# Optimization experiments

Measured on AMD Instinct MI355X. Metric: run time of the kernel, lower is better.

Reference implementation:

```python
import jax, jax.numpy as jnp
import numpy as np

N_HEADS = 32
N_KV_HEADS = 8
HEAD_DIM = 128
HIDDEN = 4096
ROPE_BASE = 10000.0


def _rope_tables(seq_len, head_dim, base):
    inv_freq = 1.0 / (base ** (jnp.arange(0, head_dim, 2, dtype=jnp.float32) / head_dim))
    t = jnp.arange(seq_len, dtype=jnp.float32)
    freqs = jnp.outer(t, inv_freq)                    # (S, D/2)
    emb = jnp.concatenate([freqs, freqs], axis=-1)    # (S, D)
    return jnp.cos(emb), jnp.sin(emb)


def _rotate_half(x):
    half = x.shape[-1] // 2
    return jnp.concatenate([-x[..., half:], x[..., :half]], axis=-1)


def _apply_rope(x, cos, sin):
    # x: (B, H, S, D); cos/sin: (S, D)
    return x * cos[None, None] + _rotate_half(x) * sin[None, None]


def setup_inputs() -> dict:
    key = jax.random.key(0)
    k1, k2, k3 = jax.random.split(key, 3)
    bsz, q_len = 2, 2048
    total_heads = N_HEADS + 2 * N_KV_HEADS
    hidden_states = jax.random.normal(k1, (bsz, q_len, HIDDEN), dtype=jnp.float32)
    w_qkv = jax.random.normal(k2, (total_heads * HEAD_DIM, HIDDEN), dtype=jnp.float32) * 0.02
    w_o = jax.random.normal(k3, (HIDDEN, N_HEADS * HEAD_DIM), dtype=jnp.float32) * 0.02
    return {"hidden_states": hidden_states, "w_qkv": w_qkv, "w_o": w_o}


def reference(hidden_states, w_qkv, w_o):
    bsz, q_len, _ = hidden_states.shape
    n_rep = N_HEADS // N_KV_HEADS

    qkv = jnp.einsum('bsh,oh->bso', hidden_states, w_qkv)  # (B, S, total_heads*D)
    q_sz = N_HEADS * HEAD_DIM
    kv_sz = N_KV_HEADS * HEAD_DIM
    q = qkv[..., :q_sz].reshape(bsz, q_len, N_HEADS, HEAD_DIM).transpose(0, 2, 1, 3)
    k = qkv[..., q_sz:q_sz + kv_sz].reshape(bsz, q_len, N_KV_HEADS, HEAD_DIM).transpose(0, 2, 1, 3)
    v = qkv[..., q_sz + kv_sz:].reshape(bsz, q_len, N_KV_HEADS, HEAD_DIM).transpose(0, 2, 1, 3)

    cos, sin = _rope_tables(q_len, HEAD_DIM, ROPE_BASE)
    q = _apply_rope(q, cos, sin)
    k = _apply_rope(k, cos, sin)

    # repeat KV heads for GQA
    k = jnp.repeat(k, n_rep, axis=1)  # (B, H, S, D)
    v = jnp.repeat(v, n_rep, axis=1)

    scale = HEAD_DIM ** -0.5
    scores = jnp.einsum('bhqd,bhkd->bhqk', q, k) * scale
    causal = jnp.tril(jnp.ones((q_len, q_len), dtype=bool))
    scores = jnp.where(causal[None, None], scores, jnp.finfo(scores.dtype).min)
    attn = jax.nn.softmax(scores, axis=-1)
    out = jnp.einsum('bhqk,bhkd->bhqd', attn, v)  # (B, H, S, D)
    out = out.transpose(0, 2, 1, 3).reshape(bsz, q_len, N_HEADS * HEAD_DIM)
    return jnp.einsum('bso,ho->bsh', out, w_o)
```

## Files before the change

kernel.cpp:

```cpp
#include <hip/hip_runtime.h>
#include <stdint.h>

#define N_HEADS   32
#define N_KV      8
#define HEAD_DIM  128
#define HIDDEN_DIM 4096
#define BSZ       2
#define SEQ       2048
#define TOT_HEADS 48
#define QKV_DIM   6144
#define ROWS      4096
#define ROPE_HEADS 40

typedef __attribute__((ext_vector_type(4)))  float f32x4;
typedef __attribute__((ext_vector_type(16))) float f32x16;
typedef __attribute__((ext_vector_type(8)))  short bf16x8;
typedef unsigned short u16;
typedef unsigned int   u32;

#define AS1 __attribute__((address_space(1)))
#define AS3 __attribute__((address_space(3)))

static __device__ __forceinline__ float bf16f(u16 u) { return __uint_as_float(((u32)u) << 16); }
static __device__ __forceinline__ u16 f2bf(float f) {
  u32 x = __float_as_uint(f);
  x += 0x7fffu + ((x >> 16) & 1u);
  return (u16)(x >> 16);
}
static __device__ __forceinline__ u32 cvt_pk_bf16(float lo, float hi) {
  u32 r;
  asm("v_cvt_pk_bf16_f32 %0, %1, %2" : "=v"(r) : "v"(lo), "v"(hi));
  return r;
}
static __device__ __forceinline__ bf16x8 mk8(u32 a, u32 b, u32 c, u32 d) {
  union { u32 u[4]; bf16x8 v; } x;
  x.u[0] = a; x.u[1] = b; x.u[2] = c; x.u[3] = d;
  return x.v;
}

#define SBAR()  do { __builtin_amdgcn_sched_barrier(0); __builtin_amdgcn_s_barrier(); \
                     __builtin_amdgcn_sched_barrier(0); } while (0)
#define LGKM0() do { asm volatile("s_waitcnt lgkmcnt(0)" ::: "memory"); \
                     __builtin_amdgcn_sched_barrier(0); } while (0)

__global__ void cast3_k(const float4* __restrict__ a, const float4* __restrict__ b,
                        const float4* __restrict__ c,
                        ushort4* __restrict__ oa, ushort4* __restrict__ ob,
                        ushort4* __restrict__ oc, int na, int nb, int nc) {
  int i = blockIdx.x * blockDim.x + threadIdx.x;
  const int stride = gridDim.x * blockDim.x;
  const int tot = na + nb + nc;
  for (; i < tot; i += stride) {
    const float4* s; ushort4* d; int j = i;
    if (j < na)           { s = a; d = oa; }
    else if (j < na + nb) { s = b; d = ob; j -= na; }
    else                  { s = c; d = oc; j -= na + nb; }
    const float4 v = s[j];
    ushort4 o;
    o.x = f2bf(v.x); o.y = f2bf(v.y); o.z = f2bf(v.z); o.w = f2bf(v.w);
    d[j] = o;
  }
}

__global__ void rope_tables_k(float* __restrict__ ctab, float* __restrict__ stab) {
  int t = blockIdx.x * blockDim.x + threadIdx.x;
  if (t >= SEQ * 64) return;
  int s = t >> 6, i = t & 63;
  float inv = powf(10000.0f, -(float)i / 64.0f);
  float ang = (float)s * inv;
  float sv, cv;
  sincosf(ang, &sv, &cv);
  ctab[t] = cv; stab[t] = sv;
}

template<int F32OUT>
__global__ __launch_bounds__(512, 2)
void gemm256_k(const u16* __restrict__ A, const u16* __restrict__ Bw,
               void* __restrict__ C, int M, int N, int K)
{
  extern __shared__ uint4 lds[];
  uint4* LA = lds;
  uint4* LB = lds + 4096;
  const int NT = K >> 6;
  const int tid  = threadIdx.x;
  const int lane = tid & 63;
  const int wave = tid >> 6;
  const int nbx = N >> 8;
  const int cpx = gridDim.x >> 3;
  const int wg  = (blockIdx.x & 7) * cpx + (blockIdx.x >> 3);
  const int bm = (wg / nbx) << 8;
  const int bn = (wg % nbx) << 8;

  const int wm = (wave >> 2) << 7;
  const int wn = (wave & 3) << 6;
  const int fr = lane & 15;
  const int fq = lane >> 4;
  const int s7 = fr & 7;

  const int rA  = (wave << 3) + (lane >> 3);
  const int c8e = (((lane & 7) ^ (lane >> 3)) << 3);

  auto SA = [&](int t, int h, int buf) {
    uint4* d = LA + (buf << 11) + (h << 10) + (wave << 6);
    const u16* s = A + (size_t)(bm + (h << 7) + rA) * K + (t << 6) + c8e;
    __builtin_amdgcn_global_load_lds((const AS1 u32*)s, (AS3 u32*)d, 16, 0, 0);
    __builtin_amdgcn_global_load_lds((const AS1 u32*)(s + (size_t)64 * K), (AS3 u32*)(d + 512), 16, 0, 0);
  };
  auto SB = [&](int t, int h, int buf) {
    uint4* d = LB + (buf << 11) + (h << 10) + (wave << 6);
    const u16* s = Bw + (size_t)(bn + (h << 7) + rA) * K + (t << 6) + c8e;
    __builtin_amdgcn_global_load_lds((const AS1 u32*)s, (AS3 u32*)d, 16, 0, 0);
    __builtin_amdgcn_global_load_lds((const AS1 u32*)(s + (size_t)64 * K), (AS3 u32*)(d + 512), 16, 0, 0);
  };

  f32x4 acc[8][4];
#pragma unroll
  for (int m = 0; m < 8; ++m)
#pragma unroll
    for (int n = 0; n < 4; ++n)
      acc[m][n] = {0.f, 0.f, 0.f, 0.f};

  SB(0, 0, 0); SB(0, 1, 0); SA(0, 0, 0); SA(0, 1, 0);
  SB(1, 0, 1); SB(1, 1, 1); SA(1, 0, 1);
  asm volatile("s_waitcnt vmcnt(6)" ::: "memory");
  SBAR();

  bf16x8 Af[4][2], B0[2][2], B1[2][2];

#pragma unroll 1
  for (int t = 0; t < NT; ++t) {
    const int buf  = t & 1;
    const int base = buf << 11;
    const int abase = base + ((wm + fr) << 3);
    const int bbase = base + ((wn + fr) << 3);

#pragma unroll
    for (int m = 0; m < 4; ++m)
#pragma unroll
      for (int kk = 0; kk < 2; ++kk)
        Af[m][kk] = *reinterpret_cast<const bf16x8*>(&LA[abase + m * 128 + (((kk << 2) + fq) ^ s7)]);
#pragma unroll
    for (int n = 0; n < 2; ++n)
#pragma unroll
      for (int kk = 0; kk < 2; ++kk)
        B0[n][kk] = *reinterpret_cast<const bf16x8*>(&LB[bbase + n * 128 + (((kk << 2) + fq) ^ s7)]);
    if (t + 1 < NT) SA(t + 1, 1, buf ^ 1);
    SBAR();
    LGKM0();
    __builtin_amdgcn_s_setprio(1);
#pragma unroll
    for (int m = 0; m < 4; ++m)
#pragma unroll
      for (int n = 0; n < 2; ++n)
#pragma unroll
        for (int kk = 0; kk < 2; ++kk)
          acc[m][n] = __builtin_amdgcn_mfma_f32_16x16x32_bf16(Af[m][kk], B0[n][kk], acc[m][n], 0, 0, 0);
    __builtin_amdgcn_s_setprio(0);
    SBAR();

#pragma unroll
    for (int n = 0; n < 2; ++n)
#pragma unroll
      for (int kk = 0; kk < 2; ++kk)
        B1[n][kk] = *reinterpret_cast<const bf16x8*>(&LB[bbase + (2 + n) * 128 + (((kk << 2) + fq) ^ s7)]);
    SBAR();
    LGKM0();
    __builtin_amdgcn_s_setprio(1);
#pragma unroll
    for (int m = 0; m < 4; ++m)
#pragma unroll
      for (int n = 0; n < 2; ++n)
#pragma unroll
        for (int kk = 0; kk < 2; ++kk)
          acc[m][2 + n] = __builtin_amdgcn_mfma_f32_16x16x32_bf16(Af[m][kk], B1[n][kk], acc[m][2 + n], 0, 0, 0);
    __builtin_amdgcn_s_setprio(0);
    SBAR();

#pragma unroll
    for (int m = 0; m < 4; ++m)
#pragma unroll
      for (int kk = 0; kk < 2; ++kk)
        Af[m][kk] = *reinterpret_cast<const bf16x8*>(&LA[abase + 512 + m * 128 + (((kk << 2) + fq) ^ s7)]);
    if (t + 2 < NT) SB(t + 2, 0, buf);
    SBAR();
    LGKM0();
    __builtin_amdgcn_s_setprio(1);
#pragma unroll
    for (int m = 0; m < 4; ++m)
#pragma unroll
      for (int n = 0; n < 2; ++n)
#pragma unroll
        for (int kk = 0; kk < 2; ++kk)
          acc[4 + m][2 + n] = __builtin_amdgcn_mfma_f32_16x16x32_bf16(Af[m][kk], B1[n][kk], acc[4 + m][2 + n], 0, 0, 0);
    __builtin_amdgcn_s_setprio(0);
    SBAR();

    if (t + 2 < NT) { SB(t + 2, 1, buf); SA(t + 2, 0, buf); }
    __builtin_amdgcn_s_setprio(1);
#pragma unroll
    for (int m = 0; m < 4; ++m)
#pragma unroll
      for (int n = 0; n < 2; ++n)
#pragma unroll
        for (int kk = 0; kk < 2; ++kk)
          acc[4 + m][n] = __builtin_amdgcn_mfma_f32_16x16x32_bf16(Af[m][kk], B0[n][kk], acc[4 + m][n], 0, 0, 0);
    __builtin_amdgcn_s_setprio(0);
    if (t < NT - 2)       { asm volatile("s_waitcnt vmcnt(6)" ::: "memory"); }
    else if (t == NT - 2) { asm volatile("s_waitcnt vmcnt(0)" ::: "memory"); }
    SBAR();
  }

  const int col0 = bn + wn + fr;
#pragma unroll
  for (int m = 0; m < 8; ++m) {
#pragma unroll
    for (int i = 0; i < 4; ++i) {
      const int row = bm + wm + (m << 4) + (fq << 2) + i;
      if (F32OUT) {
        float* rp = reinterpret_cast<float*>(C) + (size_t)row * N + col0;
#pragma unroll
        for (int n = 0; n < 4; ++n) rp[n << 4] = acc[m][n][i];
      } else {
        u16* rp = reinterpret_cast<u16*>(C) + (size_t)row * N + col0;
#pragma unroll
        for (int n = 0; n < 4; ++n) rp[n << 4] = f2bf(acc[m][n][i]);
      }
    }
  }
}

__global__ void rope_scatter_k(const u16* __restrict__ QKV,
                               const float* __restrict__ ctab, const float* __restrict__ stab,
                               u16* __restrict__ Qo, u16* __restrict__ Ko)
{
  const int t = blockIdx.x * blockDim.x + threadIdx.x;
  const int d = t & 63;
  const int hh = (t >> 6) % ROPE_HEADS;
  const int row = t / (64 * ROPE_HEADS);
  const int b = row >> 11, sq = row & (SEQ - 1);
  const u16* src = QKV + (size_t)row * QKV_DIM + hh * HEAD_DIM;
  const float x1 = bf16f(src[d]);
  const float x2 = bf16f(src[d + 64]);
  const float c = ctab[(sq << 6) + d], sn = stab[(sq << 6) + d];
  float y1 = x1 * c - x2 * sn;
  float y2 = x2 * c + x1 * sn;
  u16* dst;
  if (hh < N_HEADS) {
    const float SC2 = 0.1275170747f;
    y1 *= SC2; y2 *= SC2;
    dst = Qo + ((size_t)(b * N_HEADS + hh) * SEQ + sq) * HEAD_DIM;
  } else {
    dst = Ko + ((size_t)(b * N_KV + (hh - N_HEADS)) * SEQ + sq) * HEAD_DIM;
  }
  dst[d] = f2bf(y1);
  dst[d + 64] = f2bf(y2);
}

__global__ __launch_bounds__(256)
void vtrans_k(const u16* __restrict__ QKV, u16* __restrict__ Vt)
{
  __shared__ u16 tile[64][72];
  const int idx = blockIdx.x;
  const int dt = idx & 1;
  const int st = (idx >> 1) & 31;
  const int kv = (idx >> 6) & 7;
  const int b  = idx >> 9;
  const int tid = threadIdx.x;
  const int s0 = st << 6, d0 = dt << 6;
  const int rl = tid >> 3, cc8 = (tid & 7) << 3;
#pragma unroll
  for (int p = 0; p < 2; ++p) {
    const int sl = rl + (p << 5);
    const u16* src = QKV + (size_t)(b * SEQ + s0 + sl) * QKV_DIM
                   + (N_HEADS + N_KV + kv) * HEAD_DIM + d0 + cc8;
    *reinterpret_cast<uint4*>(&tile[sl][cc8]) = *reinterpret_cast<const uint4*>(src);
  }
  __syncthreads();
#pragma unroll
  for (int p = 0; p < 2; ++p) {
    const int dl = rl + (p << 5);
    u16 tmp[8];
#pragma unroll
    for (int k2 = 0; k2 < 8; ++k2) tmp[k2] = tile[cc8 + k2][dl];
    u16* dst = Vt + ((size_t)(b * N_KV + kv) * HEAD_DIM + d0 + dl) * SEQ + s0 + cc8;
    *reinterpret_cast<uint4*>(dst) = *reinterpret_cast<const uint4*>(tmp);
  }
}

__global__ __launch_bounds__(512, 2)
void attn_mfma_k(const u16* __restrict__ Q, const u16* __restrict__ K,
                 const u16* __restrict__ Vt, u16* __restrict__ Out)
{
  __shared__ uint4 Ksm[2][512];
  __shared__ uint4 Vsm[2][512];
  const int tid  = threadIdx.x;
  const int lane = tid & 63;
  const int w    = tid >> 6;
  const int idx  = blockIdx.x;
  const int kvh  = idx & 7;
  const int b    = (idx >> 3) & 1;
  const int qi   = 31 - (idx >> 4);
  const int q0   = qi << 6;
  const int head = w & 3;
  const int qsub = w >> 2;
  const int h    = (kvh << 2) + head;
  const int diag = 2 * qi + qsub;
  const int nsub = 2 * qi + 2;

  const int ql = lane & 31;
  const int hh = lane >> 5;

  const u16* Qh = Q  + (size_t)(b * N_HEADS + h) * SEQ * HEAD_DIM;
  const u16* Kb = K  + (size_t)(b * N_KV + kvh) * SEQ * HEAD_DIM;
  const u16* Vb = Vt + (size_t)(b * N_KV + kvh) * HEAD_DIM * SEQ;

  int koff[8];
#pragma unroll
  for (int f = 0; f < 8; ++f) koff[f] = (ql << 4) + (((f << 1) + hh) ^ (ql & 15));
  int voff0[4], voff1[4];
#pragma unroll
  for (int dblk = 0; dblk < 4; ++dblk) {
    const int d = (dblk << 5) + ql;
    voff0[dblk] = (d << 2) + (hh ^ (d & 3));
    voff1[dblk] = (d << 2) + ((2 + hh) ^ (d & 3));
  }

  auto stage = [&](int buf, int ks) {
    const int sl = (w << 6) + lane;
    {
      const int row = sl >> 4, cs = sl & 15;
      const int g = cs ^ (row & 15);
      const u16* src = Kb + (size_t)(ks + row) * HEAD_DIM + (g << 3);
      __builtin_amdgcn_global_load_lds((const AS1 u32*)src, (AS3 u32*)&Ksm[buf][w << 6], 16, 0, 0);
    }
    {
      const int d = sl >> 2, cs = sl & 3;
      const int g = cs ^ (d & 3);
      const u16* src = Vb + (size_t)d * SEQ + ks + (g << 3);
      __builtin_amdgcn_global_load_lds((const AS1 u32*)src, (AS3 u32*)&Vsm[buf][w << 6], 16, 0, 0);
    }
  };

  bf16x8 qf[8];
#pragma unroll
  for (int f = 0; f < 8; ++f)
    qf[f] = *reinterpret_cast<const bf16x8*>(Qh + (size_t)(q0 + (qsub << 5) + ql) * HEAD_DIM
                                             + 16 * f + 8 * hh);

  f32x16 o[4];
#pragma unroll
  for (int dblk = 0; dblk < 4; ++dblk)
#pragma unroll
    for (int r = 0; r < 16; ++r) o[dblk][r] = 0.f;
  float m2 = -1e30f, lsum = 0.f;

  stage(0, 0);

#pragma unroll 1
  for (int s = 0; s < nsub; ++s) {
    const int cur = s & 1;
    __syncthreads();
    if (s + 1 < nsub) stage(cur ^ 1, (s + 1) << 5);

    if (s <= diag) {
      f32x16 T;
#pragma unroll
      for (int r = 0; r < 16; ++r) T[r] = 0.f;
      __builtin_amdgcn_s_setprio(1);
#pragma unroll
      for (int f = 0; f < 8; ++f) {
        const bf16x8 kf = *reinterpret_cast<const bf16x8*>(&Ksm[cur][koff[f]]);
        T = __builtin_amdgcn_mfma_f32_32x32x16_bf16(kf, qf[f], T, 0, 0, 0);
      }
      __builtin_amdgcn_s_setprio(0);

      if (s == diag) {
#pragma unroll
        for (int r = 0; r < 16; ++r) {
          const int kr = (r & 3) + ((r >> 2) << 3) + (hh << 2);
          if (kr > ql) T[r] = -1e30f;
        }
      }
      float mt = T[0];
#pragma unroll
      for (int r = 1; r < 16; ++r) mt = fmaxf(mt, T[r]);
      mt = fmaxf(mt, __shfl_xor(mt, 32));

      if (__any(mt > m2 + 8.f)) {
        const float mnew = fmaxf(m2, mt);
        const float resc = exp2f(m2 - mnew);
        lsum *= resc;
#pragma unroll
        for (int r = 0; r < 16; ++r) {
          const int qr = (r & 3) + ((r >> 2) << 3) + (hh << 2);
          const float rr = __shfl(resc, qr);
#pragma unroll
          for (int dblk = 0; dblk < 4; ++dblk) o[dblk][r] *= rr;
        }
        m2 = mnew;
      }

      float ps = 0.f;
#pragma unroll
      for (int r = 0; r < 16; ++r) { const float pv = exp2f(T[r] - m2); T[r] = pv; ps += pv; }
      ps += __shfl_xor(ps, 32);
      lsum += ps;

      u32 pk[8], sw[8];
#pragma unroll
      for (int i = 0; i < 8; ++i) {
        pk[i] = cvt_pk_bf16(T[2 * i], T[2 * i + 1]);
        sw[i] = (u32)__shfl_xor((int)pk[i], 32);
      }
      const bf16x8 a0 = hh ? mk8(sw[2], sw[3], pk[2], pk[3])
                           : mk8(pk[0], pk[1], sw[0], sw[1]);
      const bf16x8 a1 = hh ? mk8(sw[6], sw[7], pk[6], pk[7])
                           : mk8(pk[4], pk[5], sw[4], sw[5]);

      __builtin_amdgcn_s_setprio(1);
#pragma unroll
      for (int dblk = 0; dblk < 4; ++dblk) {
        const bf16x8 va = *reinterpret_cast<const bf16x8*>(&Vsm[cur][voff0[dblk]]);
        o[dblk] = __builtin_amdgcn_mfma_f32_32x32x16_bf16(a0, va, o[dblk], 0, 0, 0);
        const bf16x8 vb2 = *reinterpret_cast<const bf16x8*>(&Vsm[cur][voff1[dblk]]);
        o[dblk] = __builtin_amdgcn_mfma_f32_32x32x16_bf16(a1, vb2, o[dblk], 0, 0, 0);
      }
      __builtin_amdgcn_s_setprio(0);
    }
  }

  u16* Ob = Out + (size_t)(b * SEQ + q0 + (qsub << 5)) * HIDDEN_DIM + h * HEAD_DIM + ql;
#pragma unroll
  for (int r = 0; r < 16; ++r) {
    const int qr = (r & 3) + ((r >> 2) << 3) + (hh << 2);
    const float il = 1.0f / __shfl(lsum, qr);
    u16* rp = Ob + (size_t)qr * HIDDEN_DIM;
#pragma unroll
    for (int dblk = 0; dblk < 4; ++dblk)
      rp[dblk * 32] = f2bf(o[dblk][r] * il);
  }
}

extern "C" void kernel_launch(void* const* d_in, const int* in_sizes, int n_in,
                              void* d_out, int out_size, void* d_ws, size_t ws_size,
                              hipStream_t stream)
{
  const float* hs   = (const float*)d_in[0];
  const float* wqkv = (const float*)d_in[1];
  const float* wo   = (const float*)d_in[2];
  float* out = (float*)d_out;
  char* ws = (char*)d_ws;
  size_t off = 0;
  auto alloc = [&](size_t bytes) -> void* {
    void* p = ws + off;
    off += (bytes + 255) & ~(size_t)255;
    return p;
  };
  u16* Xbf    = (u16*)alloc((size_t)ROWS * HIDDEN_DIM * 2);
  u16* Wqkvbf = (u16*)alloc((size_t)QKV_DIM * HIDDEN_DIM * 2);
  u16* Wobf   = (u16*)alloc((size_t)HIDDEN_DIM * HIDDEN_DIM * 2);
  u16* QKVbf  = (u16*)alloc((size_t)ROWS * QKV_DIM * 2);
  u16* Qbf    = (u16*)alloc((size_t)BSZ * N_HEADS * SEQ * HEAD_DIM * 2);
  u16* Kbf    = (u16*)alloc((size_t)BSZ * N_KV * SEQ * HEAD_DIM * 2);
  u16* Vtbf   = (u16*)alloc((size_t)BSZ * N_KV * SEQ * HEAD_DIM * 2);
  float* ctab = (float*)alloc((size_t)SEQ * 64 * 4);
  float* stab = (float*)alloc((size_t)SEQ * 64 * 4);
  u16* AOut   = (u16*)alloc((size_t)ROWS * HIDDEN_DIM * 2);
  if (off > ws_size) return;

  (void)hipFuncSetAttribute(reinterpret_cast<const void*>(&gemm256_k<0>),
                            hipFuncAttributeMaxDynamicSharedMemorySize, 131072);
  (void)hipFuncSetAttribute(reinterpret_cast<const void*>(&gemm256_k<1>),
                            hipFuncAttributeMaxDynamicSharedMemorySize, 131072);

  cast3_k<<<4096, 256, 0, stream>>>((const float4*)hs, (const float4*)wqkv, (const float4*)wo,
                                    (ushort4*)Xbf, (ushort4*)Wqkvbf, (ushort4*)Wobf,
                                    ROWS * HIDDEN_DIM / 4, QKV_DIM * HIDDEN_DIM / 4,
                                    HIDDEN_DIM * HIDDEN_DIM / 4);
  rope_tables_k<<<(SEQ * 64) / 256, 256, 0, stream>>>(ctab, stab);

  gemm256_k<0><<<(ROWS / 256) * (QKV_DIM / 256), 512, 131072, stream>>>(Xbf, Wqkvbf, (void*)QKVbf,
                                                                        ROWS, QKV_DIM, HIDDEN_DIM);
  rope_scatter_k<<<ROWS * ROPE_HEADS * 64 / 256, 256, 0, stream>>>(QKVbf, ctab, stab, Qbf, Kbf);
  vtrans_k<<<BSZ * N_KV * (SEQ / 64) * (HEAD_DIM / 64), 256, 0, stream>>>(QKVbf, Vtbf);
  attn_mfma_k<<<BSZ * N_KV * (SEQ / 64), 512, 0, stream>>>(Qbf, Kbf, Vtbf, AOut);
  gemm256_k<1><<<(ROWS / 256) * (HIDDEN_DIM / 256), 512, 131072, stream>>>(AOut, Wobf, (void*)out,
                                                                           ROWS, HIDDEN_DIM, HIDDEN_DIM);
}
```

Baseline: 545.6 us.

## Use a 128x128-tile single-buffered GEMM kernel for the QKV projection

Adds a new bf16 MFMA GEMM with 128x128 tiles, 256 threads, static 32KB shared memory, XOR-swizzled LDS and direct global-to-LDS loads. The QKV projection now uses it in place of the 256x256-tile kernel. This yields more workgroups (1536 vs 384) for better CU occupancy on the 4096x6144 output. In exchange it loses the larger kernel's data reuse and any double-buffering, with a sync after each K step.

```diff
diff --git a/kernel.cpp b/kernel.cpp
--- a/kernel.cpp
+++ b/kernel.cpp
@@ -71,6 +71,89 @@
   float sv, cv;
   sincosf(ang, &sv, &cv);
   ctab[t] = cv; stab[t] = sv;
+}
+
+template<int F32OUT>
+__global__ __launch_bounds__(256, 2)
+void gemm_bt_k(const u16* __restrict__ A, const u16* __restrict__ Bw,
+               void* __restrict__ C, int M, int N, int K)
+{
+  __shared__ uint4 smA[1024];
+  __shared__ uint4 smB[1024];
+  const int tid = threadIdx.x;
+  const int nbx = N >> 7;
+  const int cpx = gridDim.x >> 3;
+  const int wg  = (blockIdx.x & 7) * cpx + (blockIdx.x >> 3);
+  const int bm = (wg / nbx) << 7;
+  const int bn = (wg % nbx) << 7;
+  const int lane = tid & 63;
+  const int wave = tid >> 6;
+  const int wm = (wave >> 1) << 6;
+  const int wn = (wave & 1) << 6;
+  const int fr = lane & 15;
+  const int fq = lane >> 4;
+
+  f32x4 acc[4][4];
+#pragma unroll
+  for (int i = 0; i < 4; ++i)
+#pragma unroll
+    for (int j = 0; j < 4; ++j)
+      acc[i][j] = {0.f, 0.f, 0.f, 0.f};
+
+  const int gl_r = lane >> 3;
+  const int gl_c = (lane & 7) ^ gl_r;
+
+  for (int k0 = 0; k0 < K; k0 += 64) {
+#pragma unroll
+    for (int i = 0; i < 4; ++i) {
+      const int rbase = (wave << 5) + (i << 3);
+      const int row = rbase + gl_r;
+      const u16* gA = A  + (size_t)(bm + row) * K + k0 + (gl_c << 3);
+      const u16* gB = Bw + (size_t)(bn + row) * K + k0 + (gl_c << 3);
+      __builtin_amdgcn_global_load_lds((const AS1 u32*)gA, (AS3 u32*)&smA[rbase << 3], 16, 0, 0);
+      __builtin_amdgcn_global_load_lds((const AS1 u32*)gB, (AS3 u32*)&smB[rbase << 3], 16, 0, 0);
+    }
+    __syncthreads();
+#pragma unroll
+    for (int kk = 0; kk < 2; ++kk) {
+      bf16x8 af[4], bfr[4];
+      const int cc = (kk << 2) + fq;
+#pragma unroll
+      for (int m = 0; m < 4; ++m) {
+        const int row = wm + (m << 4) + fr;
+        af[m] = *reinterpret_cast<const bf16x8*>(&smA[(row << 3) + (cc ^ (row & 7))]);
+      }
+#pragma unroll
+      for (int n = 0; n < 4; ++n) {
+        const int row = wn + (n << 4) + fr;
+        bfr[n] = *reinterpret_cast<const bf16x8*>(&smB[(row << 3) + (cc ^ (row & 7))]);
+      }
+#pragma unroll
+      for (int m = 0; m < 4; ++m)
+#pragma unroll
+        for (int n = 0; n < 4; ++n)
+          acc[m][n] = __builtin_amdgcn_mfma_f32_16x16x32_bf16(af[m], bfr[n], acc[m][n], 0, 0, 0);
+    }
+    __syncthreads();
+  }
+
+  const int col0 = bn + wn + fr;
+#pragma unroll
+  for (int m = 0; m < 4; ++m) {
+#pragma unroll
+    for (int i = 0; i < 4; ++i) {
+      const int row = bm + wm + (m << 4) + (fq << 2) + i;
+      if (F32OUT) {
+        float* rp = reinterpret_cast<float*>(C) + (size_t)row * N + col0;
+#pragma unroll
+        for (int n = 0; n < 4; ++n) rp[n << 4] = acc[m][n][i];
+      } else {
+        u16* rp = reinterpret_cast<u16*>(C) + (size_t)row * N + col0;
+#pragma unroll
+        for (int n = 0; n < 4; ++n) rp[n << 4] = f2bf(acc[m][n][i]);
+      }
+    }
+  }
 }
 
 template<int F32OUT>
@@ -468,8 +551,6 @@
   u16* AOut   = (u16*)alloc((size_t)ROWS * HIDDEN_DIM * 2);
   if (off > ws_size) return;
 
-  (void)hipFuncSetAttribute(reinterpret_cast<const void*>(&gemm256_k<0>),
-                            hipFuncAttributeMaxDynamicSharedMemorySize, 131072);
   (void)hipFuncSetAttribute(reinterpret_cast<const void*>(&gemm256_k<1>),
                             hipFuncAttributeMaxDynamicSharedMemorySize, 131072);
 
@@ -479,8 +560,8 @@
                                     HIDDEN_DIM * HIDDEN_DIM / 4);
   rope_tables_k<<<(SEQ * 64) / 256, 256, 0, stream>>>(ctab, stab);
 
-  gemm256_k<0><<<(ROWS / 256) * (QKV_DIM / 256), 512, 131072, stream>>>(Xbf, Wqkvbf, (void*)QKVbf,
-                                                                        ROWS, QKV_DIM, HIDDEN_DIM);
+  gemm_bt_k<0><<<(ROWS / 128) * (QKV_DIM / 128), 256, 0, stream>>>(Xbf, Wqkvbf, (void*)QKVbf,
+                                                                   ROWS, QKV_DIM, HIDDEN_DIM);
   rope_scatter_k<<<ROWS * ROPE_HEADS * 64 / 256, 256, 0, stream>>>(QKVbf, ctab, stab, Qbf, Kbf);
   vtrans_k<<<BSZ * N_KV * (SEQ / 64) * (HEAD_DIM / 64), 256, 0, stream>>>(QKVbf, Vtbf);
   attn_mfma_k<<<BSZ * N_KV * (SEQ / 64), 512, 0, stream>>>(Qbf, Kbf, Vtbf, AOut);
```

Measured after the change: 588.1 us. 1.08x slower.
